# Kernel optimization log

Hardware: AMD Instinct MI355X
Metric: run time of the kernel (lower is better)

Reference implementation:

```python
import jax, jax.numpy as jnp
import numpy as np

H = 16          # num_heads
NB = 32         # pos_bias_num_buckets
EPS = 1e-8      # RMSNorm eps


def setup_inputs() -> dict:
    key = jax.random.key(0)
    ks = jax.random.split(key, 8)
    B, L, K, R, M, Dm, Dq = 2, 32, 2, 64, 128, 2048, 2048
    x = jax.random.normal(ks[0], (B, L, K, R, Dm), jnp.float32)
    past_ca_hidden_states = jax.random.normal(ks[1], (B, L, M, Dm), jnp.float32)
    past_ca_attention_mask = jax.random.bernoulli(ks[2], 0.95, (B, L, M)).astype(jnp.float32)
    ln_scale = jnp.ones((Dm,), jnp.float32)
    q_w = jax.random.normal(ks[3], (Dq, Dm), jnp.float32) * 0.02      # torch Linear weight [out,in]
    kv_w = jax.random.normal(ks[4], (2 * Dq, Dm), jnp.float32) * 0.02
    out_w = jax.random.normal(ks[5], (Dm, Dq), jnp.float32) * 0.02
    bias_table = jax.random.normal(ks[6], (NB, H), jnp.float32) * 0.02  # relative_attention_bias.weight
    return dict(x=x, past_ca_hidden_states=past_ca_hidden_states,
                past_ca_attention_mask=past_ca_attention_mask,
                ln_scale=ln_scale, q_w=q_w, kv_w=kv_w, out_w=out_w,
                bias_table=bias_table)


def _rel_bias(bias_table, r, m):
    # linear bucketing, bidirectional=True (RelativePositionBias._relative_position_bucket_linear)
    mn = -(NB // 2) - (NB % 2 - 1)   # -15 for NB=32
    mx = NB // 2                      # 16
    rel = jnp.arange(m)[None, :] - jnp.arange(r)[:, None]   # memory - query, [r, m]
    buckets = jnp.clip(rel, mn, mx) - mn                    # in [0, NB)
    return jnp.transpose(bias_table[buckets], (2, 0, 1))    # [H, r, m]


def reference(x, past_ca_hidden_states, past_ca_attention_mask,
              ln_scale, q_w, kv_w, out_w, bias_table):
    B, L, K, R, Dm = x.shape
    M = past_ca_hidden_states.shape[2]
    Dq = q_w.shape[0]
    dh = Dq // H

    # RMSNorm (p=-1: full norm)
    rms = jnp.linalg.norm(x, axis=-1, keepdims=True) * (Dm ** -0.5)
    xn = (x / (rms + EPS)) * ln_scale

    # projections (no bias)
    q = jnp.einsum('blkrc,qc->blkrq', xn, q_w)                 # [B,L,K,R,Dq]
    kv = jnp.einsum('blmc,qc->blmq', past_ca_hidden_states, kv_w)  # [B,L,M,2Dq]
    k = kv[..., :Dq]
    v = kv[..., Dq:]

    # split heads
    q = q.reshape(B, L, K, R, H, dh).transpose(0, 1, 2, 4, 3, 5)  # [B,L,K,H,R,dh]
    k = k.reshape(B, L, M, H, dh).transpose(0, 1, 3, 2, 4)        # [B,L,H,M,dh]
    v = v.reshape(B, L, M, H, dh).transpose(0, 1, 3, 2, 4)        # [B,L,H,M,dh]

    # NOTE: original applies NO 1/sqrt(dh) scaling
    scores = jnp.einsum('blkhrd,blhmd->blkhrm', q, k)             # [B,L,K,H,R,M]
    scores = scores + _rel_bias(bias_table, R, M)                 # broadcast [H,R,M]
    mask_add = (1.0 - past_ca_attention_mask) * -10000.0          # [B,L,M]
    scores = scores + mask_add[:, :, None, None, None, :]

    attn = jax.nn.softmax(scores, axis=-1)
    out = jnp.einsum('blkhrm,blhmd->blkhrd', attn, v)             # [B,L,K,H,R,dh]
    out = out.transpose(0, 1, 2, 4, 3, 5).reshape(B, L, K, R, Dq)  # merge heads '(h d)'
    out = jnp.einsum('blkrq,cq->blkrc', out, out_w)                # final_proj
    return out + x, attn
```

## Files before the change

kernel.cpp:

```cpp
#include <hip/hip_runtime.h>

typedef _Float16 f16;
typedef _Float16 f16x8 __attribute__((ext_vector_type(8)));
typedef float f32x4 __attribute__((ext_vector_type(4)));

#define LDS_GL16(g, l) __builtin_amdgcn_global_load_lds( \
    (const __attribute__((address_space(1))) void*)(g),  \
    (__attribute__((address_space(3))) void*)(l), 16, 0, 0)
#define VMCNT(N) asm volatile("s_waitcnt vmcnt(" #N ")" ::: "memory")
#define BAR() __builtin_amdgcn_s_barrier()

__global__ __launch_bounds__(256) void conv4_kern(
        const float* __restrict__ s0, f16* __restrict__ d0,
        const float* __restrict__ s1, f16* __restrict__ d1,
        const float* __restrict__ s2, f16* __restrict__ d2,
        const float* __restrict__ s3, f16* __restrict__ d3) {
    int b = blockIdx.x;
    const float* in; f16* out; long base;
    if (b < 2048)       { in = s0; out = d0; base = (long)b * 2048; }
    else if (b < 6144)  { in = s1; out = d1; base = (long)(b - 2048) * 2048; }
    else if (b < 8192)  { in = s2; out = d2; base = (long)(b - 6144) * 2048; }
    else                { in = s3; out = d3; base = (long)(b - 8192) * 2048; }
    long o = base + threadIdx.x * 8;
    float4 a = *(const float4*)(in + o);
    float4 c = *(const float4*)(in + o + 4);
    f16x8 v = { (f16)a.x,(f16)a.y,(f16)a.z,(f16)a.w,
                (f16)c.x,(f16)c.y,(f16)c.z,(f16)c.w };
    *(f16x8*)(out + o) = v;
}

__global__ __launch_bounds__(256) void rmsnorm_kern(const float* __restrict__ x,
                                                    const float* __restrict__ scale,
                                                    f16* __restrict__ out) {
    long base = (long)blockIdx.x * 2048 + threadIdx.x * 8;
    float4 a = *(const float4*)(x + base);
    float4 b = *(const float4*)(x + base + 4);
    float ss = a.x*a.x + a.y*a.y + a.z*a.z + a.w*a.w
             + b.x*b.x + b.y*b.y + b.z*b.z + b.w*b.w;
    #pragma unroll
    for (int d = 1; d < 64; d <<= 1) ss += __shfl_xor(ss, d, 64);
    __shared__ float red[4];
    if ((threadIdx.x & 63) == 0) red[threadIdx.x >> 6] = ss;
    __syncthreads();
    ss = red[0] + red[1] + red[2] + red[3];
    float inv = 1.0f / (sqrtf(ss * (1.0f / 2048.0f)) + 1e-8f);
    int c = threadIdx.x * 8;
    float4 s1 = *(const float4*)(scale + c);
    float4 s2 = *(const float4*)(scale + c + 4);
    f16x8 v = { (f16)(a.x*inv*s1.x),(f16)(a.y*inv*s1.y),(f16)(a.z*inv*s1.z),(f16)(a.w*inv*s1.w),
                (f16)(b.x*inv*s2.x),(f16)(b.y*inv*s2.y),(f16)(b.z*inv*s2.z),(f16)(b.w*inv*s2.w) };
    *(f16x8*)(out + base) = v;
}

template<int EPI>
__global__ __launch_bounds__(512, 2) void gemm256(
        const f16* __restrict__ A, const f16* __restrict__ B,
        f16* __restrict__ Ch, float* __restrict__ Cf,
        const float* __restrict__ resid, int M, int N, int Kd) {
    alignas(16) __shared__ f16 lds[65536];
    int nbx = N >> 8;
    int cpx = gridDim.x >> 3;
    int fid = (blockIdx.x & 7) * cpx + (blockIdx.x >> 3);
    int by = fid / nbx, bx = fid % nbx;
    int m0 = by << 8, n0 = bx << 8;
    int tid = threadIdx.x, lane = tid & 63;
    int wid = tid >> 6, wm = wid >> 2, wn = wid & 3;
    int lr = lane & 15, g = lane >> 4;
    int iL = tid >> 3, cb = tid & 7;

    long goff[8]; int doff[8];
    {
        #pragma unroll
        for (int rd = 0; rd < 2; ++rd) {
            int rA0 = iL + rd * 128;
            goff[0 + rd] = (long)(m0 + rA0) * Kd + ((cb ^ (rA0 & 7)) << 3);
            doff[0 + rd] = rA0 * 64 + cb * 8;
            int rB0 = (iL & 31) + ((iL >> 5) + rd * 2) * 64;
            goff[2 + rd] = (long)(n0 + rB0) * Kd + ((cb ^ (rB0 & 7)) << 3);
            doff[2 + rd] = 32768 + rB0 * 64 + cb * 8;
            int rB1 = rB0 + 32;
            goff[4 + rd] = (long)(n0 + rB1) * Kd + ((cb ^ (rB1 & 7)) << 3);
            doff[4 + rd] = 32768 + rB1 * 64 + cb * 8;
            int rA1 = rA0 + 64;
            goff[6 + rd] = (long)(m0 + rA1) * Kd + ((cb ^ (rA1 & 7)) << 3);
            doff[6 + rd] = rA1 * 64 + cb * 8;
        }
    }
    auto stage = [&](int kt, int p, int r) {
        const f16* src = (r == 0 || r == 3) ? A : B;
        #pragma unroll
        for (int rd = 0; rd < 2; ++rd)
            LDS_GL16(src + goff[r * 2 + rd] + kt * 64,
                     lds + p * 16384 + doff[r * 2 + rd]);
    };

    const char* ldsc = (const char*)lds;
    int swz = lr & 7;
    const char* baseA[2], *baseB[2];
    baseA[0] = ldsc + (wm * 128 + lr) * 128 + ((g ^ swz) << 4);
    baseA[1] = ldsc + (wm * 128 + lr) * 128 + (((4 + g) ^ swz) << 4);
    baseB[0] = ldsc + 65536 + (wn * 64 + lr) * 128 + ((g ^ swz) << 4);
    baseB[1] = ldsc + 65536 + (wn * 64 + lr) * 128 + (((4 + g) ^ swz) << 4);

    f32x4 acc[8][4] = {};
    f16x8 a[4][2], b0[2][2], b1[2][2];

    auto loadA = [&](int bufB, int qm) {
        #pragma unroll
        for (int mf = 0; mf < 4; ++mf)
            #pragma unroll
            for (int kk = 0; kk < 2; ++kk)
                a[mf][kk] = *(const f16x8*)(baseA[kk] + bufB + qm * 8192 + mf * 2048);
    };
    auto loadB = [&](f16x8 (&d)[2][2], int bufB, int qn) {
        #pragma unroll
        for (int nf = 0; nf < 2; ++nf)
            #pragma unroll
            for (int kk = 0; kk < 2; ++kk)
                d[nf][kk] = *(const f16x8*)(baseB[kk] + bufB + qn * 4096 + nf * 2048);
    };
    auto mma = [&](f16x8 (&bb)[2][2], int qm, int qn) {
        __builtin_amdgcn_s_setprio(1);
        #pragma unroll
        for (int kk = 0; kk < 2; ++kk)
            #pragma unroll
            for (int mf = 0; mf < 4; ++mf)
                #pragma unroll
                for (int nf = 0; nf < 2; ++nf)
                    acc[qm * 4 + mf][qn * 2 + nf] = __builtin_amdgcn_mfma_f32_16x16x32_f16(
                        a[mf][kk], bb[nf][kk], acc[qm * 4 + mf][qn * 2 + nf], 0, 0, 0);
        __builtin_amdgcn_s_setprio(0);
    };

    int NT = Kd >> 6, NI = NT >> 1;

    stage(0, 0, 0); stage(0, 0, 1); stage(0, 0, 2); stage(0, 0, 3);
    stage(1, 1, 0); stage(1, 1, 1); stage(1, 1, 2);
    VMCNT(6); BAR();

    for (int it = 0; it < NI - 1; ++it) {
        int t0 = it * 2;
        loadA(0, 0); loadB(b0, 0, 0);
        stage(t0 + 1, 1, 3);
        BAR(); mma(b0, 0, 0); BAR();
        loadB(b1, 0, 1);
        stage(t0 + 2, 0, 0);
        BAR(); mma(b1, 0, 1); BAR();
        loadA(0, 1);
        stage(t0 + 2, 0, 1);
        BAR(); mma(b1, 1, 1); BAR();
        stage(t0 + 2, 0, 2);
        VMCNT(6);
        BAR(); mma(b0, 1, 0); BAR();
        loadA(32768, 0); loadB(b0, 32768, 0);
        stage(t0 + 2, 0, 3);
        BAR(); mma(b0, 0, 0); BAR();
        loadB(b1, 32768, 1);
        stage(t0 + 3, 1, 0);
        BAR(); mma(b1, 0, 1); BAR();
        loadA(32768, 1);
        stage(t0 + 3, 1, 1);
        BAR(); mma(b1, 1, 1); BAR();
        stage(t0 + 3, 1, 2);
        VMCNT(6);
        BAR(); mma(b0, 1, 0); BAR();
    }
    {
        loadA(0, 0); loadB(b0, 0, 0);
        stage(NT - 1, 1, 3);
        BAR(); mma(b0, 0, 0); BAR();
        loadB(b1, 0, 1);
        BAR(); mma(b1, 0, 1); BAR();
        loadA(0, 1);
        BAR(); mma(b1, 1, 1); BAR();
        VMCNT(0);
        BAR(); mma(b0, 1, 0); BAR();
        loadA(32768, 0); loadB(b0, 32768, 0);
        BAR(); mma(b0, 0, 0); BAR();
        loadB(b1, 32768, 1);
        BAR(); mma(b1, 0, 1); BAR();
        loadA(32768, 1);
        BAR(); mma(b1, 1, 1); BAR();
        BAR(); mma(b0, 1, 0);
    }

    #pragma unroll
    for (int i = 0; i < 8; ++i) {
        #pragma unroll
        for (int j = 0; j < 4; ++j) {
            #pragma unroll
            for (int reg = 0; reg < 4; ++reg) {
                int row = m0 + wm * 128 + i * 16 + g * 4 + reg;
                int col = n0 + wn * 64 + j * 16 + lr;
                long idx = (long)row * N + col;
                float v = acc[i][j][reg];
                if (EPI == 0) Ch[idx] = (f16)v;
                else          Cf[idx] = v + resid[idx];
            }
        }
    }
}

__global__ __launch_bounds__(256, 2) void attn_kern(
        const f16* __restrict__ Q,
        const f16* __restrict__ KV,
        const float* __restrict__ mask,
        const float* __restrict__ bias,
        float* __restrict__ attn_out,
        f16* __restrict__ pv_out) {
    __shared__ f16 Vs[128 * 128];
    __shared__ f16 P[64 * 136];
    int blk = blockIdx.x;
    int h  = blk & 15;
    int bk = blk >> 4;
    int bl = bk >> 1;
    int tid = threadIdx.x, lane = tid & 63, w = tid >> 6;
    int r0 = w << 4;
    int lr = lane & 15, g = lane >> 4;
    long qbase  = (long)bk * 64 * 2048;
    long kvbase = (long)bl * 128 * 4096;
    const f16* vsrc = KV + kvbase + 2048 + h * 128;
    {
        int idx = tid;
        #pragma unroll
        for (int rnd = 0; rnd < 8; ++rnd) {
            int vrow = idx >> 4, c = idx & 15;
            LDS_GL16(vsrc + (long)vrow * 4096 + c * 8, Vs + idx * 8);
            idx += 256;
        }
    }
    f16x8 aq[4];
    const f16* qrow = Q + qbase + (long)(r0 + lr) * 2048 + h * 128 + g * 8;
    #pragma unroll
    for (int t4 = 0; t4 < 4; ++t4) aq[t4] = *(const f16x8*)(qrow + t4 * 32);
    f32x4 s[8] = {};
    const f16* kbase = KV + kvbase + h * 128 + g * 8;
    #pragma unroll
    for (int j = 0; j < 8; ++j) {
        #pragma unroll
        for (int t4 = 0; t4 < 4; ++t4) {
            f16x8 bkf = *(const f16x8*)(kbase + (long)(j * 16 + lr) * 4096 + t4 * 32);
            s[j] = __builtin_amdgcn_mfma_f32_16x16x32_f16(aq[t4], bkf, s[j], 0, 0, 0);
        }
    }
    float madd[8];
    #pragma unroll
    for (int j = 0; j < 8; ++j)
        madd[j] = (1.0f - mask[(long)bl * 128 + j * 16 + lr]) * -10000.0f;
    #pragma unroll
    for (int reg = 0; reg < 4; ++reg) {
        int r = r0 + g * 4 + reg;
        float mx = -3.0e38f;
        #pragma unroll
        for (int j = 0; j < 8; ++j) {
            int m = j * 16 + lr;
            int rel = m - r;
            int bkt = (rel < -15 ? -15 : (rel > 16 ? 16 : rel)) + 15;
            float v = s[j][reg] + bias[bkt * 16 + h] + madd[j];
            s[j][reg] = v;
            mx = fmaxf(mx, v);
        }
        #pragma unroll
        for (int d = 1; d < 16; d <<= 1) mx = fmaxf(mx, __shfl_xor(mx, d, 64));
        float sum = 0.0f;
        #pragma unroll
        for (int j = 0; j < 8; ++j) {
            float e = __expf(s[j][reg] - mx);
            s[j][reg] = e;
            sum += e;
        }
        #pragma unroll
        for (int d = 1; d < 16; d <<= 1) sum += __shfl_xor(sum, d, 64);
        float inv = 1.0f / sum;
        #pragma unroll
        for (int j = 0; j < 8; ++j) s[j][reg] *= inv;
    }
    long abase = (long)blk * 64 * 128;
    #pragma unroll
    for (int reg = 0; reg < 4; ++reg) {
        int r = r0 + g * 4 + reg;
        #pragma unroll
        for (int j = 0; j < 8; ++j) {
            attn_out[abase + (long)r * 128 + j * 16 + lr] = s[j][reg];
            P[r * 136 + j * 16 + lr] = (f16)s[j][reg];
        }
    }
    __syncthreads();
    f16x8 pa[4];
    #pragma unroll
    for (int t4 = 0; t4 < 4; ++t4)
        pa[t4] = *(const f16x8*)(P + (r0 + lr) * 136 + t4 * 32 + g * 8);
    f32x4 o[8] = {};
    #pragma unroll
    for (int dj = 0; dj < 8; ++dj) {
        #pragma unroll
        for (int t4 = 0; t4 < 4; ++t4) {
            f16x8 bv;
            #pragma unroll
            for (int rg = 0; rg < 8; ++rg)
                bv[rg] = Vs[(t4 * 32 + g * 8 + rg) * 128 + dj * 16 + lr];
            o[dj] = __builtin_amdgcn_mfma_f32_16x16x32_f16(pa[t4], bv, o[dj], 0, 0, 0);
        }
    }
    f16* ob = pv_out + qbase + h * 128;
    #pragma unroll
    for (int dj = 0; dj < 8; ++dj)
        #pragma unroll
        for (int reg = 0; reg < 4; ++reg)
            ob[(long)(r0 + g * 4 + reg) * 2048 + dj * 16 + lr] = (f16)o[dj][reg];
}

extern "C" void kernel_launch(void* const* d_in, const int* in_sizes, int n_in,
                              void* d_out, int out_size, void* d_ws, size_t ws_size,
                              hipStream_t stream) {
    const float* x     = (const float*)d_in[0];
    const float* hid   = (const float*)d_in[1];
    const float* mask  = (const float*)d_in[2];
    const float* lnsc  = (const float*)d_in[3];
    const float* q_w   = (const float*)d_in[4];
    const float* kv_w  = (const float*)d_in[5];
    const float* out_w = (const float*)d_in[6];
    const float* bias  = (const float*)d_in[7];
    float* out0 = (float*)d_out;
    float* attn = out0 + 16777216;

    f16* kv_h  = (f16*)out0;
    f16* xn_h  = (f16*)attn;
    f16* hid_h = (f16*)(attn + 8388608);
    char* ws = (char*)d_ws;
    f16* q_h    = (f16*)(ws);
    f16* ao_h   = (f16*)(ws + 33554432L);
    f16* qw_h   = (f16*)(ws + 67108864L);
    f16* kvw_h  = (f16*)(ws + 75497472L);
    f16* outw_h = (f16*)(ws + 92274688L);

    conv4_kern<<<16384, 256, 0, stream>>>(q_w, qw_h, kv_w, kvw_h,
                                          out_w, outw_h, hid, hid_h);
    rmsnorm_kern<<<8192, 256, 0, stream>>>(x, lnsc, xn_h);
    gemm256<0><<<256, 512, 0, stream>>>(xn_h, qw_h, q_h, nullptr, nullptr,
                                        8192, 2048, 2048);
    gemm256<0><<<512, 512, 0, stream>>>(hid_h, kvw_h, kv_h, nullptr, nullptr,
                                        8192, 4096, 2048);
    attn_kern<<<2048, 256, 0, stream>>>(q_h, kv_h, mask, bias, attn, ao_h);
    gemm256<1><<<256, 512, 0, stream>>>(ao_h, outw_h, nullptr, out0, x,
                                        8192, 2048, 2048);
}
```

Before: 385.2 us.

## Stage GEMM and attention epilogues through LDS and merge Q/KV GEMM launches

```diff
diff --git a/kernel.cpp b/kernel.cpp
--- a/kernel.cpp
+++ b/kernel.cpp
@@ -53,38 +53,31 @@
 }
 
 template<int EPI>
-__global__ __launch_bounds__(512, 2) void gemm256(
+__device__ __forceinline__ void gemm256_body(
         const f16* __restrict__ A, const f16* __restrict__ B,
         f16* __restrict__ Ch, float* __restrict__ Cf,
-        const float* __restrict__ resid, int M, int N, int Kd) {
+        const float* __restrict__ resid, int N, int Kd, int m0, int n0) {
     alignas(16) __shared__ f16 lds[65536];
-    int nbx = N >> 8;
-    int cpx = gridDim.x >> 3;
-    int fid = (blockIdx.x & 7) * cpx + (blockIdx.x >> 3);
-    int by = fid / nbx, bx = fid % nbx;
-    int m0 = by << 8, n0 = bx << 8;
     int tid = threadIdx.x, lane = tid & 63;
     int wid = tid >> 6, wm = wid >> 2, wn = wid & 3;
     int lr = lane & 15, g = lane >> 4;
     int iL = tid >> 3, cb = tid & 7;
 
     long goff[8]; int doff[8];
-    {
-        #pragma unroll
-        for (int rd = 0; rd < 2; ++rd) {
-            int rA0 = iL + rd * 128;
-            goff[0 + rd] = (long)(m0 + rA0) * Kd + ((cb ^ (rA0 & 7)) << 3);
-            doff[0 + rd] = rA0 * 64 + cb * 8;
-            int rB0 = (iL & 31) + ((iL >> 5) + rd * 2) * 64;
-            goff[2 + rd] = (long)(n0 + rB0) * Kd + ((cb ^ (rB0 & 7)) << 3);
-            doff[2 + rd] = 32768 + rB0 * 64 + cb * 8;
-            int rB1 = rB0 + 32;
-            goff[4 + rd] = (long)(n0 + rB1) * Kd + ((cb ^ (rB1 & 7)) << 3);
-            doff[4 + rd] = 32768 + rB1 * 64 + cb * 8;
-            int rA1 = rA0 + 64;
-            goff[6 + rd] = (long)(m0 + rA1) * Kd + ((cb ^ (rA1 & 7)) << 3);
-            doff[6 + rd] = rA1 * 64 + cb * 8;
-        }
+    #pragma unroll
+    for (int rd = 0; rd < 2; ++rd) {
+        int rA0 = iL + rd * 128;
+        goff[0 + rd] = (long)(m0 + rA0) * Kd + ((cb ^ (rA0 & 7)) << 3);
+        doff[0 + rd] = rA0 * 64 + cb * 8;
+        int rB0 = (iL & 31) + ((iL >> 5) + rd * 2) * 64;
+        goff[2 + rd] = (long)(n0 + rB0) * Kd + ((cb ^ (rB0 & 7)) << 3);
+        doff[2 + rd] = 32768 + rB0 * 64 + cb * 8;
+        int rB1 = rB0 + 32;
+        goff[4 + rd] = (long)(n0 + rB1) * Kd + ((cb ^ (rB1 & 7)) << 3);
+        doff[4 + rd] = 32768 + rB1 * 64 + cb * 8;
+        int rA1 = rA0 + 64;
+        goff[6 + rd] = (long)(m0 + rA1) * Kd + ((cb ^ (rA1 & 7)) << 3);
+        doff[6 + rd] = rA1 * 64 + cb * 8;
     }
     auto stage = [&](int kt, int p, int r) {
         const f16* src = (r == 0 || r == 3) ? A : B;
@@ -184,21 +177,74 @@
         BAR(); mma(b0, 1, 0);
     }
 
-    #pragma unroll
-    for (int i = 0; i < 8; ++i) {
-        #pragma unroll
-        for (int j = 0; j < 4; ++j) {
-            #pragma unroll
-            for (int reg = 0; reg < 4; ++reg) {
-                int row = m0 + wm * 128 + i * 16 + g * 4 + reg;
-                int col = n0 + wn * 64 + j * 16 + lr;
-                long idx = (long)row * N + col;
-                float v = acc[i][j][reg];
-                if (EPI == 0) Ch[idx] = (f16)v;
-                else          Cf[idx] = v + resid[idx];
+    __syncthreads();
+    if (EPI == 0) {
+        #pragma unroll
+        for (int i = 0; i < 8; ++i)
+            #pragma unroll
+            for (int j = 0; j < 4; ++j)
+                #pragma unroll
+                for (int reg = 0; reg < 4; ++reg)
+                    lds[(wm * 128 + i * 16 + g * 4 + reg) * 256 + wn * 64 + j * 16 + lr] =
+                        (f16)acc[i][j][reg];
+        __syncthreads();
+        #pragma unroll
+        for (int k = 0; k < 16; ++k) {
+            int e = k * 4096 + tid * 8;
+            int row = e >> 8, col = e & 255;
+            *(f16x8*)(Ch + (long)(m0 + row) * N + n0 + col) = *(const f16x8*)(lds + e);
+        }
+    } else {
+        float* Ct = (float*)lds;
+        #pragma unroll
+        for (int h = 0; h < 2; ++h) {
+            if (h) __syncthreads();
+            if (wm == h) {
+                #pragma unroll
+                for (int i = 0; i < 8; ++i)
+                    #pragma unroll
+                    for (int j = 0; j < 4; ++j)
+                        #pragma unroll
+                        for (int reg = 0; reg < 4; ++reg)
+                            Ct[(i * 16 + g * 4 + reg) * 256 + wn * 64 + j * 16 + lr] =
+                                acc[i][j][reg];
             }
-        }
-    }
+            __syncthreads();
+            #pragma unroll
+            for (int k = 0; k < 8; ++k) {
+                int e = k * 4096 + tid * 8;
+                int row = e >> 8, col = e & 255;
+                long gi = (long)(m0 + h * 128 + row) * N + n0 + col;
+                float4 c0 = *(const float4*)(Ct + e);
+                float4 c1 = *(const float4*)(Ct + e + 4);
+                float4 r0 = *(const float4*)(resid + gi);
+                float4 r1 = *(const float4*)(resid + gi + 4);
+                c0.x += r0.x; c0.y += r0.y; c0.z += r0.z; c0.w += r0.w;
+                c1.x += r1.x; c1.y += r1.y; c1.z += r1.z; c1.w += r1.w;
+                *(float4*)(Cf + gi) = c0;
+                *(float4*)(Cf + gi + 4) = c1;
+            }
+        }
+    }
+}
+
+__global__ __launch_bounds__(512, 2) void gemm_qkv(
+        const f16* __restrict__ Aq, const f16* __restrict__ Bq, f16* __restrict__ Cq,
+        const f16* __restrict__ Akv, const f16* __restrict__ Bkv, f16* __restrict__ Ckv) {
+    int fid = (blockIdx.x & 7) * 96 + (blockIdx.x >> 3);
+    const f16 *A, *B; f16* C; int N, lf, sh;
+    if (fid < 256) { A = Aq;  B = Bq;  C = Cq;  N = 2048; lf = fid;       sh = 3; }
+    else           { A = Akv; B = Bkv; C = Ckv; N = 4096; lf = fid - 256; sh = 4; }
+    int by = lf >> sh, bx = lf & ((1 << sh) - 1);
+    gemm256_body<0>(A, B, C, nullptr, nullptr, N, 2048, by << 8, bx << 8);
+}
+
+__global__ __launch_bounds__(512, 2) void gemm_out(
+        const f16* __restrict__ A, const f16* __restrict__ B,
+        float* __restrict__ Cf, const float* __restrict__ resid) {
+    int fid = (blockIdx.x & 7) * 32 + (blockIdx.x >> 3);
+    int by = fid >> 3, bx = fid & 7;
+    gemm256_body<1>(A, B, nullptr, Cf, resid, 2048, 2048, by << 8, bx << 8);
 }
 
 __global__ __launch_bounds__(256, 2) void attn_kern(
@@ -302,12 +348,20 @@
             o[dj] = __builtin_amdgcn_mfma_f32_16x16x32_f16(pa[t4], bv, o[dj], 0, 0, 0);
         }
     }
+    __syncthreads();
+    #pragma unroll
+    for (int dj = 0; dj < 8; ++dj)
+        #pragma unroll
+        for (int reg = 0; reg < 4; ++reg)
+            Vs[(r0 + g * 4 + reg) * 128 + dj * 16 + lr] = (f16)o[dj][reg];
+    __syncthreads();
     f16* ob = pv_out + qbase + h * 128;
     #pragma unroll
-    for (int dj = 0; dj < 8; ++dj)
-        #pragma unroll
-        for (int reg = 0; reg < 4; ++reg)
-            ob[(long)(r0 + g * 4 + reg) * 2048 + dj * 16 + lr] = (f16)o[dj][reg];
+    for (int k = 0; k < 4; ++k) {
+        int e = k * 2048 + tid * 8;
+        int row = e >> 7, col = e & 127;
+        *(f16x8*)(ob + (long)row * 2048 + col) = *(const f16x8*)(Vs + e);
+    }
 }
 
 extern "C" void kernel_launch(void* const* d_in, const int* in_sizes, int n_in,
@@ -337,11 +391,7 @@
     conv4_kern<<<16384, 256, 0, stream>>>(q_w, qw_h, kv_w, kvw_h,
                                           out_w, outw_h, hid, hid_h);
     rmsnorm_kern<<<8192, 256, 0, stream>>>(x, lnsc, xn_h);
-    gemm256<0><<<256, 512, 0, stream>>>(xn_h, qw_h, q_h, nullptr, nullptr,
-                                        8192, 2048, 2048);
-    gemm256<0><<<512, 512, 0, stream>>>(hid_h, kvw_h, kv_h, nullptr, nullptr,
-                                        8192, 4096, 2048);
+    gemm_qkv<<<768, 512, 0, stream>>>(xn_h, qw_h, q_h, hid_h, kvw_h, kv_h);
     attn_kern<<<2048, 256, 0, stream>>>(q_h, kv_h, mask, bias, attn, ao_h);
-    gemm256<1><<<256, 512, 0, stream>>>(ao_h, outw_h, nullptr, out0, x,
-                                        8192, 2048, 2048);
-}
+    gemm_out<<<256, 512, 0, stream>>>(ao_h, outw_h, out0, x);
+}
```

Result: faster. 375.9 us (-2.4%).
